# Optimization experiments

Hardware: AMD Instinct MI355X
Metric: run time of the kernel (lower is better)

The kernel has to match this reference:

```python
import jax, jax.numpy as jnp
import numpy as np

NUM_HEADS = 12
TOPK = 4


def setup_inputs() -> dict:
    key = jax.random.key(0)
    ks = jax.random.split(key, 5)
    B, N, C = 32, 577, 768
    s = 0.02
    return {
        "x": jax.random.normal(ks[0], (B, N, C), jnp.float32),
        "qkv_w": jax.random.normal(ks[1], (3 * C, C), jnp.float32) * s,
        "qkv_b": jax.random.normal(ks[2], (3 * C,), jnp.float32) * s,
        "proj_w": jax.random.normal(ks[3], (C, C), jnp.float32) * s,
        "proj_b": jax.random.normal(ks[4], (C,), jnp.float32) * s,
    }


def reference(x, qkv_w, qkv_b, proj_w, proj_b):
    B, N, C = x.shape
    H = NUM_HEADS
    D = C // H
    scale = D ** -0.5  # 0.125, matches original_attention.scale

    # qkv projection: (B,N,3C) -> (3,B,H,N,D)
    qkv = (x @ qkv_w.T + qkv_b).reshape(B, N, 3, H, D).transpose(2, 0, 3, 1, 4)
    q, k, v = qkv[0], qkv[1], qkv[2]

    # heuristic head routing: mean squared query energy per head
    scores = jnp.mean(q.astype(jnp.float32) ** 2, axis=(0, 2, 3))  # (H,)
    _, idx = jax.lax.top_k(scores, TOPK)
    idx = jnp.sort(idx)  # (topk,)

    q_sel = q[:, idx]  # (B,topk,N,D)
    k_sel = k[:, idx]
    v_sel = v[:, idx]

    attn = jax.nn.softmax(jnp.einsum('bhnd,bhmd->bhnm', q_sel, k_sel) * scale, axis=-1)
    y_sel = jnp.einsum('bhnm,bhmd->bhnd', attn, v_sel)  # (B,topk,N,D)

    # scatter selected heads back into full-size tensors (as in the torch module)
    y_full = jnp.zeros((B, H, N, D), x.dtype).at[:, idx].set(y_sel)
    x_out = y_full.transpose(0, 2, 1, 3).reshape(B, N, C) @ proj_w.T + proj_b

    attn_full = jnp.zeros((B, H, N, N), x.dtype).at[:, idx].set(attn)
    return x_out, attn_full
```

## Files before the change

### kernel.cpp

```cpp
#include <hip/hip_runtime.h>
#include <hip/hip_bf16.h>
#include <stdint.h>
#include <stddef.h>

#define B_ 32
#define N_ 577
#define C_ 768
#define H_ 12
#define D_ 64
#define M_ (B_*N_)
#define K3_ (3*C_)
#define NP_ 640
#define NN_ (N_*N_)

typedef __bf16 bf16x8_t __attribute__((ext_vector_type(8)));
typedef float f32x4 __attribute__((ext_vector_type(4)));
typedef unsigned short u16x8 __attribute__((ext_vector_type(8)));
typedef unsigned short u16x4 __attribute__((ext_vector_type(4)));

static __device__ __forceinline__ f32x4 mfma16(u16x8 a, u16x8 b, f32x4 c) {
  return __builtin_amdgcn_mfma_f32_16x16x32_bf16(
      __builtin_bit_cast(bf16x8_t, a), __builtin_bit_cast(bf16x8_t, b), c, 0, 0, 0);
}

static __device__ __forceinline__ unsigned short f2bf(float x) {
  unsigned int u = __builtin_bit_cast(unsigned int, x);
  u += 0x7fffu + ((u >> 16) & 1u);
  return (unsigned short)(u >> 16);
}

static __device__ __forceinline__ void glds16(const unsigned short* g, unsigned short* l) {
  __builtin_amdgcn_global_load_lds(
      (__attribute__((address_space(1))) void*)g,
      (__attribute__((address_space(3))) void*)l,
      16, 0, 0);
}

static __device__ __forceinline__ void top4sel(const float* __restrict__ scores, int* sel) {
  float s[H_];
  #pragma unroll
  for (int i = 0; i < H_; ++i) s[i] = scores[i];
  #pragma unroll
  for (int t = 0; t < 4; ++t) {
    int best = 0; float bv = s[0];
    #pragma unroll
    for (int i = 1; i < H_; ++i)
      if (s[i] > bv) { bv = s[i]; best = i; }
    sel[t] = best;
    #pragma unroll
    for (int i = 0; i < H_; ++i)
      s[i] = (i == best) ? -3.0e38f : s[i];
  }
  #pragma unroll
  for (int a = 0; a < 4; ++a)
    #pragma unroll
    for (int b2 = a + 1; b2 < 4; ++b2)
      if (sel[b2] < sel[a]) { int t = sel[a]; sel[a] = sel[b2]; sel[b2] = t; }
}

__global__ void k_cvt2(const float* __restrict__ srcx, unsigned short* __restrict__ dstx, int n4x,
                       const float* __restrict__ srcw, unsigned short* __restrict__ dstw, int n4w,
                       float* __restrict__ zeroptr) {
  if (blockIdx.x == 0 && threadIdx.x < 16) zeroptr[threadIdx.x] = 0.f;
  const float* src; unsigned short* dst; int n4, i0, stride;
  if (blockIdx.x < 2048) {
    src = srcx; dst = dstx; n4 = n4x;
    i0 = blockIdx.x * 256 + threadIdx.x; stride = 2048 * 256;
  } else {
    src = srcw; dst = dstw; n4 = n4w;
    i0 = (blockIdx.x - 2048) * 256 + threadIdx.x; stride = 512 * 256;
  }
  for (int i = i0; i < n4; i += stride) {
    float4 v = ((const float4*)src)[i];
    u16x4 o;
    o[0] = f2bf(v.x); o[1] = f2bf(v.y); o[2] = f2bf(v.z); o[3] = f2bf(v.w);
    *(u16x4*)(dst + (size_t)i * 4) = o;
  }
}

#define ZPER_ 146948
template<int MODE>
__global__ void k_gemm(const unsigned short* __restrict__ A,
                       const unsigned short* __restrict__ Bm,
                       const float* __restrict__ bias,
                       unsigned short* __restrict__ qb,
                       unsigned short* __restrict__ kb,
                       unsigned short* __restrict__ vb,
                       float* __restrict__ scores,
                       float* __restrict__ out,
                       int Mtot, int Ktot)
{
  __shared__ unsigned short As[128 * 32];
  __shared__ unsigned short Bs[128 * 32];
  const int tid = threadIdx.x;
  int bn;

  if (MODE == 0) {
    const int y = blockIdx.y;
    if ((y & 3) == 0) {
      const int zblk = (y >> 2) * 145 + blockIdx.x;
      const size_t Z = (size_t)B_ * H_ * NN_;
      size_t s0 = (size_t)zblk * ZPER_;
      size_t len = ZPER_;
      if (s0 + len > Z) len = Z - s0;
      float* zo = out + s0;
      const float4 z4 = {0.f, 0.f, 0.f, 0.f};
      for (size_t t = tid * 4; t + 4 <= len; t += 4096)
        *(float4*)(zo + t) = z4;
      return;
    }
    bn = y - 1 - (y >> 2);
  } else {
    bn = blockIdx.y;
  }

  const int bm = blockIdx.x;
  const int w = tid >> 6, l = tid & 63;
  const int wm = w >> 1, wn = w & 1;
  const int lr = l & 15, lg = l >> 4;
  const int lk = lg * 8;
  f32x4 acc[4][4] = {};
  const int rowA0 = bm * 128, rowB0 = bn * 128;
  const int le0 = w * 1024 + l * 8;
  const int kiters = Ktot >> 5;
  for (int kt = 0; kt < kiters; ++kt) {
    __syncthreads();
    #pragma unroll
    for (int c = 0; c < 2; ++c) {
      int lea = le0 + c * 512;
      int ra = lea >> 5, ka = lea & 31;
      glds16(A  + (size_t)(rowA0 + ra) * Ktot + kt * 32 + ka, As + (w * 2 + c) * 512);
      glds16(Bm + (size_t)(rowB0 + ra) * Ktot + kt * 32 + ka, Bs + (w * 2 + c) * 512);
    }
    __syncthreads();
    u16x8 af[4], bfr[4];
    #pragma unroll
    for (int i = 0; i < 4; ++i)
      af[i] = *(const u16x8*)(As + (wm * 64 + i * 16 + lr) * 32 + lk);
    #pragma unroll
    for (int j = 0; j < 4; ++j)
      bfr[j] = *(const u16x8*)(Bs + (wn * 64 + j * 16 + lr) * 32 + lk);
    #pragma unroll
    for (int i = 0; i < 4; ++i)
      #pragma unroll
      for (int j = 0; j < 4; ++j)
        acc[i][j] = mfma16(af[i], bfr[j], acc[i][j]);
  }

  const int rbase = lg * 4;
  if (MODE == 0) {
    const int n0 = rowB0 + wn * 64;
    const int t0 = n0 / C_;
    const int h0 = (n0 % C_) >> 6;
    unsigned short* dstbuf = (t0 == 0) ? qb : ((t0 == 1) ? kb : vb);
    float bs[4];
    #pragma unroll
    for (int j = 0; j < 4; ++j) bs[j] = bias[n0 + j * 16 + lr];
    float sq = 0.f;
    #pragma unroll
    for (int i = 0; i < 4; ++i) {
      const int mbase = rowA0 + wm * 64 + i * 16 + rbase;
      const int bb0 = mbase / N_;
      const int np0 = mbase - bb0 * N_;
      #pragma unroll
      for (int r = 0; r < 4; ++r) {
        const int mm = mbase + r;
        if (mm < Mtot) {
          int np = np0 + r, bb = bb0;
          if (np >= N_) { np -= N_; bb += 1; }
          unsigned short* drow = dstbuf + (((size_t)(bb * H_ + h0)) * N_ + np) * D_;
          #pragma unroll
          for (int j = 0; j < 4; ++j) {
            const float v = acc[i][j][r] + bs[j];
            if (t0 == 0) sq += v * v;
            drow[j * 16 + lr] = f2bf(v);
          }
        }
      }
    }
    if (t0 == 0) {
      #pragma unroll
      for (int s2 = 1; s2 < 64; s2 <<= 1) sq += __shfl_xor(sq, s2);
      if (l == 0) atomicAdd(scores + h0, sq);
    }
  } else {
    #pragma unroll
    for (int j = 0; j < 4; ++j) {
      const int n = rowB0 + wn * 64 + j * 16 + lr;
      const float bsj = bias[n];
      #pragma unroll
      for (int i = 0; i < 4; ++i) {
        const int mbase = rowA0 + wm * 64 + i * 16 + rbase;
        #pragma unroll
        for (int r = 0; r < 4; ++r) {
          const int mm = mbase + r;
          if (mm < Mtot) out[(size_t)mm * C_ + n] = acc[i][j][r] + bsj;
        }
      }
    }
  }
}

__global__ void k_prep(const unsigned short* __restrict__ vb, unsigned short* __restrict__ vT,
                       const float* __restrict__ scores,
                       const float* __restrict__ pw, unsigned short* __restrict__ pwsel) {
  int sel[4];
  top4sel(scores, sel);
  const int bid = blockIdx.x;
  const int tid = threadIdx.x;

  if (bid >= 1280) {
    const int i = (bid - 1280) * 256 + tid;
    const int c = i >> 8, j = i & 255;
    const int h = sel[j >> 6], d = j & 63;
    pwsel[i] = f2bf(pw[(size_t)c * C_ + h * 64 + d]);
    return;
  }

  __shared__ unsigned short t[64][72];
  const int nt = bid % 10;
  const int p  = bid / 10;
  const int b  = p >> 2, hs = p & 3;
  const int h  = sel[hs];
  const size_t bh_src = (size_t)(b * H_ + h);
  const size_t bh_dst = (size_t)(b * 4 + hs);
  const int n0 = nt * 64;
  {
    const int r = tid >> 2, q4 = (tid & 3) * 16;
    const int n = n0 + r;
    u16x8 v0, v1;
    if (n < N_) {
      const unsigned short* src = vb + (bh_src * N_ + n) * D_ + q4;
      v0 = *(const u16x8*)(src);
      v1 = *(const u16x8*)(src + 8);
    } else {
      #pragma unroll
      for (int j = 0; j < 8; ++j) { v0[j] = 0; v1[j] = 0; }
    }
    *(u16x8*)&t[r][q4] = v0;
    *(u16x8*)&t[r][q4 + 8] = v1;
  }
  __syncthreads();
  {
    const int d = tid >> 2, nc = (tid & 3) * 16;
    u16x8 w0, w1;
    #pragma unroll
    for (int j = 0; j < 8; ++j) { w0[j] = t[nc + j][d]; w1[j] = t[nc + 8 + j][d]; }
    unsigned short* dst = vT + (bh_dst * D_ + d) * NP_ + n0 + nc;
    *(u16x8*)(dst) = w0;
    *(u16x8*)(dst + 8) = w1;
  }
}

__global__ void k_attn(const unsigned short* __restrict__ qb,
                       const unsigned short* __restrict__ kb,
                       const unsigned short* __restrict__ vT,
                       const float* __restrict__ scores,
                       float* __restrict__ attn_out,
                       unsigned short* __restrict__ ysel)
{
  __shared__ unsigned short Plds[4][16][72];
  int sel[4];
  top4sel(scores, sel);
  const int bid = blockIdx.x;

  const int qt = bid >> 7;
  const int pair = bid & 127;
  const int b  = pair >> 2;
  const int hs = pair & 3;
  const int h  = sel[hs];
  const int tid = threadIdx.x;
  const int w = tid >> 6, l = tid & 63;
  const int lr = l & 15, lg = l >> 4, lk = lg * 8;
  const float sc2 = 0.125f * 1.44269504f;

  const size_t bh = (size_t)(b * H_ + h);
  const unsigned short* qbase = qb + bh * ((size_t)N_ * D_);
  const unsigned short* kbase = kb + bh * ((size_t)N_ * D_);
  const unsigned short* vbase = vT + (size_t)(b * 4 + hs) * ((size_t)D_ * NP_);
  float* aout = attn_out + bh * (size_t)NN_;

  const int qrow = qt * 64 + w * 16 + lr;
  const int qrc = (qrow < N_) ? qrow : (N_ - 1);
  u16x8 qf0 = *(const u16x8*)(qbase + (size_t)qrc * D_ + lk);
  u16x8 qf1 = *(const u16x8*)(qbase + (size_t)qrc * D_ + 32 + lk);

  const unsigned short* kp576 = kbase + (size_t)576 * D_;
  u16x8 kt0 = *(const u16x8*)(kp576 + lk);
  u16x8 kt1 = *(const u16x8*)(kp576 + 32 + lk);

  float lsum[4] = {0.f, 0.f, 0.f, 0.f};

  for (int kt = 0; kt < 9; ++kt) {
    f32x4 s[4];
    #pragma unroll
    for (int cg = 0; cg < 4; ++cg) {
      const int kc = kt * 64 + cg * 16 + lr;
      const unsigned short* kp = kbase + (size_t)kc * D_;
      u16x8 k0 = *(const u16x8*)(kp + lk);
      u16x8 k1 = *(const u16x8*)(kp + 32 + lk);
      f32x4 a = {0.f, 0.f, 0.f, 0.f};
      __builtin_amdgcn_s_setprio(1);
      a = mfma16(qf0, k0, a);
      a = mfma16(qf1, k1, a);
      __builtin_amdgcn_s_setprio(0);
      s[cg] = a;
    }
    #pragma unroll
    for (int r = 0; r < 4; ++r) {
      #pragma unroll
      for (int cg = 0; cg < 4; ++cg)
        lsum[r] += exp2f(s[cg][r] * sc2);
    }
  }
  {
    f32x4 a = {0.f, 0.f, 0.f, 0.f};
    a = mfma16(qf0, kt0, a);
    a = mfma16(qf1, kt1, a);
    #pragma unroll
    for (int r = 0; r < 4; ++r)
      lsum[r] += (lr == 0) ? exp2f(a[r] * sc2) : 0.f;
  }
  #pragma unroll
  for (int x = 1; x < 16; x <<= 1)
    #pragma unroll
    for (int r = 0; r < 4; ++r)
      lsum[r] += __shfl_xor(lsum[r], x);
  float off2[4];
  #pragma unroll
  for (int r = 0; r < 4; ++r) off2[r] = __log2f(lsum[r]);

  f32x4 y[4] = {};
  const int orow0 = qt * 64 + w * 16 + lg * 4;

  for (int kt = 0; kt < 9; ++kt) {
    f32x4 s[4];
    #pragma unroll
    for (int cg = 0; cg < 4; ++cg) {
      const int kc = kt * 64 + cg * 16 + lr;
      const unsigned short* kp = kbase + (size_t)kc * D_;
      u16x8 k0 = *(const u16x8*)(kp + lk);
      u16x8 k1 = *(const u16x8*)(kp + 32 + lk);
      f32x4 a = {0.f, 0.f, 0.f, 0.f};
      __builtin_amdgcn_s_setprio(1);
      a = mfma16(qf0, k0, a);
      a = mfma16(qf1, k1, a);
      __builtin_amdgcn_s_setprio(0);
      s[cg] = a;
    }
    #pragma unroll
    for (int cg = 0; cg < 4; ++cg) {
      const int kc = kt * 64 + cg * 16 + lr;
      #pragma unroll
      for (int r = 0; r < 4; ++r) {
        const float p = exp2f(__builtin_fmaf(s[cg][r], sc2, -off2[r]));
        const int row = orow0 + r;
        if (row < N_)
          aout[(size_t)row * N_ + kc] = p;
        Plds[w][lg * 4 + r][cg * 16 + lr] = f2bf(p);
      }
    }
    u16x8 pa0 = *(const u16x8*)&Plds[w][lr][lk];
    u16x8 pa1 = *(const u16x8*)&Plds[w][lr][32 + lk];
    #pragma unroll
    for (int cg2 = 0; cg2 < 4; ++cg2) {
      const unsigned short* vp = vbase + (size_t)(cg2 * 16 + lr) * NP_ + kt * 64;
      u16x8 v0 = *(const u16x8*)(vp + lk);
      u16x8 v1 = *(const u16x8*)(vp + 32 + lk);
      __builtin_amdgcn_s_setprio(1);
      y[cg2] = mfma16(pa0, v0, y[cg2]);
      y[cg2] = mfma16(pa1, v1, y[cg2]);
      __builtin_amdgcn_s_setprio(0);
    }
  }
  {
    f32x4 a = {0.f, 0.f, 0.f, 0.f};
    a = mfma16(qf0, kt0, a);
    a = mfma16(qf1, kt1, a);
    #pragma unroll
    for (int cg = 0; cg < 4; ++cg) {
      #pragma unroll
      for (int r = 0; r < 4; ++r) {
        float p = 0.f;
        if (cg == 0) {
          const float pv = exp2f(__builtin_fmaf(a[r], sc2, -off2[r]));
          p = (lr == 0) ? pv : 0.f;
          const int row = orow0 + r;
          if (lr == 0 && row < N_)
            aout[(size_t)row * N_ + 576] = pv;
        }
        Plds[w][lg * 4 + r][cg * 16 + lr] = f2bf(p);
      }
    }
    u16x8 pa0 = *(const u16x8*)&Plds[w][lr][lk];
    u16x8 pa1 = *(const u16x8*)&Plds[w][lr][32 + lk];
    #pragma unroll
    for (int cg2 = 0; cg2 < 4; ++cg2) {
      const unsigned short* vp = vbase + (size_t)(cg2 * 16 + lr) * NP_ + 576;
      u16x8 v0 = *(const u16x8*)(vp + lk);
      u16x8 v1 = *(const u16x8*)(vp + 32 + lk);
      y[cg2] = mfma16(pa0, v0, y[cg2]);
      y[cg2] = mfma16(pa1, v1, y[cg2]);
    }
  }

  #pragma unroll
  for (int cg2 = 0; cg2 < 4; ++cg2)
    #pragma unroll
    for (int r = 0; r < 4; ++r) {
      const int row = orow0 + r;
      if (row < N_)
        ysel[((size_t)(b * N_ + row)) * 256 + hs * 64 + cg2 * 16 + lr] = f2bf(y[cg2][r]);
    }
}

extern "C" void kernel_launch(void* const* d_in, const int* in_sizes, int n_in,
                              void* d_out, int out_size, void* d_ws, size_t ws_size,
                              hipStream_t stream) {
  const float* x      = (const float*)d_in[0];
  const float* qkv_w  = (const float*)d_in[1];
  const float* qkv_b  = (const float*)d_in[2];
  const float* proj_w = (const float*)d_in[3];
  const float* proj_b = (const float*)d_in[4];

  float* xout = (float*)d_out;
  float* attn_out = (float*)d_out + (size_t)M_ * C_;

  char* ws = (char*)d_ws;
  size_t o = 0;
  unsigned short* xb    = (unsigned short*)(ws + o);
  unsigned short* vT    = (unsigned short*)(ws + o);
  o += 31457280;
  unsigned short* wqkvb = (unsigned short*)(ws + o); o += 3538944;
  unsigned short* qb    = (unsigned short*)(ws + o); o += 28360704;
  unsigned short* kb    = (unsigned short*)(ws + o); o += 28360704;
  unsigned short* vb    = (unsigned short*)(ws + o); o += 28360704;
  unsigned short* ysel  = (unsigned short*)(ws + o); o += 9453568;
  unsigned short* pwsel = (unsigned short*)(ws + o); o += 393216;
  float* scores         = (float*)(ws + o);

  k_cvt2<<<2560, 256, 0, stream>>>(x, xb, (M_ * C_) / 4,
                                   qkv_w, wqkvb, (K3_ * C_) / 4, scores);

  k_gemm<0><<<dim3(145, 24), 256, 0, stream>>>(xb, wqkvb, qkv_b,
                                               qb, kb, vb, scores, attn_out,
                                               M_, C_);

  k_prep<<<2048, 256, 0, stream>>>(vb, vT, scores, proj_w, pwsel);

  k_attn<<<1280, 256, 0, stream>>>(qb, kb, vT, scores, attn_out, ysel);

  k_gemm<1><<<dim3(145, 6), 256, 0, stream>>>(ysel, pwsel, proj_b,
                                              nullptr, nullptr, nullptr, nullptr, xout,
                                              M_, 256);
}
```

Before: 358.0 us.

## Split QKV GEMM to compute K/V only for selected heads and zero only unselected attn slabs

The fused QKV GEMM now runs in two passes. The first computes only Q, because Q is needed to find the head scores. The second computes K and V only for the four selected heads, gathering their weight rows and writing compact 4-head buffers. The second pass also zeroes only the attention-map slabs of the eight unselected heads, instead of the whole attention output that the selected heads later overwrite. This removes the GEMM work for eight unselected heads' K/V and redundant zero writes, at the cost of an extra launch and a serialization point on the score reduction.

```diff
diff --git a/kernel.cpp b/kernel.cpp
--- a/kernel.cpp
+++ b/kernel.cpp
@@ -56,6 +56,10 @@
     #pragma unroll
     for (int b2 = a + 1; b2 < 4; ++b2)
       if (sel[b2] < sel[a]) { int t = sel[a]; sel[a] = sel[b2]; sel[b2] = t; }
+}
+
+static __device__ __forceinline__ int sel_pick(const int* sel, int h) {
+  return h == 0 ? sel[0] : (h == 1 ? sel[1] : (h == 2 ? sel[2] : sel[3]));
 }
 
 __global__ void k_cvt2(const float* __restrict__ srcx, unsigned short* __restrict__ dstx, int n4x,
@@ -78,7 +82,6 @@
   }
 }
 
-#define ZPER_ 146948
 template<int MODE>
 __global__ void k_gemm(const unsigned short* __restrict__ A,
                        const unsigned short* __restrict__ Bm,
@@ -94,22 +97,39 @@
   __shared__ unsigned short Bs[128 * 32];
   const int tid = threadIdx.x;
   int bn;
-
-  if (MODE == 0) {
+  int sel[4] = {0, 1, 2, 3};
+
+  if (MODE == 2) {
+    top4sel(scores, sel);
     const int y = blockIdx.y;
-    if ((y & 3) == 0) {
-      const int zblk = (y >> 2) * 145 + blockIdx.x;
-      const size_t Z = (size_t)B_ * H_ * NN_;
-      size_t s0 = (size_t)zblk * ZPER_;
-      size_t len = ZPER_;
-      if (s0 + len > Z) len = Z - s0;
-      float* zo = out + s0;
+    if (y == 0 || y == 3) {
+      const int x = blockIdx.x;
+      if (x >= 128) return;
+      const int slab = (y == 3 ? 128 : 0) + x;
+      const int b2 = slab >> 3, hu = slab & 7;
+      int uh[8]; int u = 0;
+      #pragma unroll
+      for (int c = 0; c < H_; ++c) {
+        bool issel = (c == sel[0]) | (c == sel[1]) | (c == sel[2]) | (c == sel[3]);
+        if (!issel) { uh[u] = c; ++u; }
+      }
+      int zh = 0;
+      #pragma unroll
+      for (int u2 = 0; u2 < 8; ++u2) if (u2 == hu) zh = uh[u2];
+      float* zo = out + ((size_t)(b2 * H_ + zh)) * NN_;
+      size_t take = NN_;
+      const int mis = (int)(((uintptr_t)zo >> 2) & 3);
+      size_t head = mis ? (size_t)(4 - mis) : 0;
+      if (head > take) head = take;
+      for (size_t t = tid; t < head; t += 256) zo[t] = 0.f;
+      float* pv = zo + head; size_t nrem = take - head;
+      const size_t nv = nrem >> 2;
       const float4 z4 = {0.f, 0.f, 0.f, 0.f};
-      for (size_t t = tid * 4; t + 4 <= len; t += 4096)
-        *(float4*)(zo + t) = z4;
+      for (size_t t = tid; t < nv; t += 256) ((float4*)pv)[t] = z4;
+      for (size_t t = (nv << 2) + tid; t < nrem; t += 256) pv[t] = 0.f;
       return;
     }
-    bn = y - 1 - (y >> 2);
+    bn = y - 1 - (y > 3 ? 1 : 0);
   } else {
     bn = blockIdx.y;
   }
@@ -123,6 +143,19 @@
   const int rowA0 = bm * 128, rowB0 = bn * 128;
   const int le0 = w * 1024 + l * 8;
   const int kiters = Ktot >> 5;
+
+  int brow_c[2];
+  #pragma unroll
+  for (int c = 0; c < 2; ++c) {
+    const int ra = (le0 + c * 512) >> 5;
+    int r = rowB0 + ra;
+    if (MODE == 2) {
+      const int part = r >> 8, hsr = (r >> 6) & 3, dd = r & 63;
+      r = 768 + part * 768 + sel_pick(sel, hsr) * 64 + dd;
+    }
+    brow_c[c] = r;
+  }
+
   for (int kt = 0; kt < kiters; ++kt) {
     __syncthreads();
     #pragma unroll
@@ -130,7 +163,7 @@
       int lea = le0 + c * 512;
       int ra = lea >> 5, ka = lea & 31;
       glds16(A  + (size_t)(rowA0 + ra) * Ktot + kt * 32 + ka, As + (w * 2 + c) * 512);
-      glds16(Bm + (size_t)(rowB0 + ra) * Ktot + kt * 32 + ka, Bs + (w * 2 + c) * 512);
+      glds16(Bm + (size_t)brow_c[c] * Ktot + kt * 32 + ka, Bs + (w * 2 + c) * 512);
     }
     __syncthreads();
     u16x8 af[4], bfr[4];
@@ -148,14 +181,22 @@
   }
 
   const int rbase = lg * 4;
-  if (MODE == 0) {
+  if (MODE == 0 || MODE == 2) {
     const int n0 = rowB0 + wn * 64;
-    const int t0 = n0 / C_;
-    const int h0 = (n0 % C_) >> 6;
-    unsigned short* dstbuf = (t0 == 0) ? qb : ((t0 == 1) ? kb : vb);
+    const int blk64 = n0 >> 6;
+    unsigned short* dstbuf;
+    int hcomp;
+    int bias0;
+    if (MODE == 0) {
+      dstbuf = qb; hcomp = blk64; bias0 = n0;
+    } else {
+      const int part = blk64 >> 2, hs2 = blk64 & 3;
+      dstbuf = part ? vb : kb; hcomp = hs2;
+      bias0 = 768 + part * 768 + sel_pick(sel, hs2) * 64;
+    }
     float bs[4];
     #pragma unroll
-    for (int j = 0; j < 4; ++j) bs[j] = bias[n0 + j * 16 + lr];
+    for (int j = 0; j < 4; ++j) bs[j] = bias[bias0 + j * 16 + lr];
     float sq = 0.f;
     #pragma unroll
     for (int i = 0; i < 4; ++i) {
@@ -168,20 +209,22 @@
         if (mm < Mtot) {
           int np = np0 + r, bb = bb0;
           if (np >= N_) { np -= N_; bb += 1; }
-          unsigned short* drow = dstbuf + (((size_t)(bb * H_ + h0)) * N_ + np) * D_;
+          unsigned short* drow = (MODE == 0)
+            ? dstbuf + (((size_t)(bb * H_ + hcomp)) * N_ + np) * D_
+            : dstbuf + (((size_t)(bb * 4  + hcomp)) * N_ + np) * D_;
           #pragma unroll
           for (int j = 0; j < 4; ++j) {
             const float v = acc[i][j][r] + bs[j];
-            if (t0 == 0) sq += v * v;
+            if (MODE == 0) sq += v * v;
             drow[j * 16 + lr] = f2bf(v);
           }
         }
       }
     }
-    if (t0 == 0) {
+    if (MODE == 0) {
       #pragma unroll
       for (int s2 = 1; s2 < 64; s2 <<= 1) sq += __shfl_xor(sq, s2);
-      if (l == 0) atomicAdd(scores + h0, sq);
+      if (l == 0) atomicAdd(scores + blk64, sq);
     }
   } else {
     #pragma unroll
@@ -204,15 +247,15 @@
 __global__ void k_prep(const unsigned short* __restrict__ vb, unsigned short* __restrict__ vT,
                        const float* __restrict__ scores,
                        const float* __restrict__ pw, unsigned short* __restrict__ pwsel) {
-  int sel[4];
-  top4sel(scores, sel);
   const int bid = blockIdx.x;
   const int tid = threadIdx.x;
 
   if (bid >= 1280) {
+    int sel[4];
+    top4sel(scores, sel);
     const int i = (bid - 1280) * 256 + tid;
     const int c = i >> 8, j = i & 255;
-    const int h = sel[j >> 6], d = j & 63;
+    const int h = sel_pick(sel, j >> 6), d = j & 63;
     pwsel[i] = f2bf(pw[(size_t)c * C_ + h * 64 + d]);
     return;
   }
@@ -221,16 +264,14 @@
   const int nt = bid % 10;
   const int p  = bid / 10;
   const int b  = p >> 2, hs = p & 3;
-  const int h  = sel[hs];
-  const size_t bh_src = (size_t)(b * H_ + h);
-  const size_t bh_dst = (size_t)(b * 4 + hs);
+  const size_t bh = (size_t)(b * 4 + hs);
   const int n0 = nt * 64;
   {
     const int r = tid >> 2, q4 = (tid & 3) * 16;
     const int n = n0 + r;
     u16x8 v0, v1;
     if (n < N_) {
-      const unsigned short* src = vb + (bh_src * N_ + n) * D_ + q4;
+      const unsigned short* src = vb + (bh * N_ + n) * D_ + q4;
       v0 = *(const u16x8*)(src);
       v1 = *(const u16x8*)(src + 8);
     } else {
@@ -246,7 +287,7 @@
     u16x8 w0, w1;
     #pragma unroll
     for (int j = 0; j < 8; ++j) { w0[j] = t[nc + j][d]; w1[j] = t[nc + 8 + j][d]; }
-    unsigned short* dst = vT + (bh_dst * D_ + d) * NP_ + n0 + nc;
+    unsigned short* dst = vT + (bh * D_ + d) * NP_ + n0 + nc;
     *(u16x8*)(dst) = w0;
     *(u16x8*)(dst + 8) = w1;
   }
@@ -268,17 +309,16 @@
   const int pair = bid & 127;
   const int b  = pair >> 2;
   const int hs = pair & 3;
-  const int h  = sel[hs];
+  const int h  = sel_pick(sel, hs);
   const int tid = threadIdx.x;
   const int w = tid >> 6, l = tid & 63;
   const int lr = l & 15, lg = l >> 4, lk = lg * 8;
   const float sc2 = 0.125f * 1.44269504f;
 
-  const size_t bh = (size_t)(b * H_ + h);
-  const unsigned short* qbase = qb + bh * ((size_t)N_ * D_);
-  const unsigned short* kbase = kb + bh * ((size_t)N_ * D_);
+  const unsigned short* qbase = qb + (size_t)(b * H_ + h) * ((size_t)N_ * D_);
+  const unsigned short* kbase = kb + (size_t)(b * 4 + hs) * ((size_t)N_ * D_);
   const unsigned short* vbase = vT + (size_t)(b * 4 + hs) * ((size_t)D_ * NP_);
-  float* aout = attn_out + bh * (size_t)NN_;
+  float* aout = attn_out + (size_t)(b * H_ + h) * (size_t)NN_;
 
   const int qrow = qt * 64 + w * 16 + lr;
   const int qrc = (qrow < N_) ? qrow : (N_ - 1);
@@ -442,9 +482,13 @@
   k_cvt2<<<2560, 256, 0, stream>>>(x, xb, (M_ * C_) / 4,
                                    qkv_w, wqkvb, (K3_ * C_) / 4, scores);
 
-  k_gemm<0><<<dim3(145, 24), 256, 0, stream>>>(xb, wqkvb, qkv_b,
-                                               qb, kb, vb, scores, attn_out,
-                                               M_, C_);
+  k_gemm<0><<<dim3(145, 6), 256, 0, stream>>>(xb, wqkvb, qkv_b,
+                                              qb, kb, vb, scores, nullptr,
+                                              M_, C_);
+
+  k_gemm<2><<<dim3(145, 6), 256, 0, stream>>>(xb, wqkvb, qkv_b,
+                                              qb, kb, vb, scores, attn_out,
+                                              M_, C_);
 
   k_prep<<<2048, 256, 0, stream>>>(vb, vT, scores, proj_w, pwsel);
 
```

Measured after the change: 388.7 us. +8.6%, slower.

## Zero only unselected attention heads inside attention kernel instead of during QKV GEMM

Applied to the files above, without the earlier changes.

Before, the QKV GEMM launch carried extra blocks that zeroed the whole B×H×N×N attention output, including the four selected heads that the attention kernel then overwrites. Now the attention kernel launches extra blocks that zero only the eight unselected heads per batch, which removes about a third of the redundant zero writes and takes the zeroing out of the GEMM grid. The cost is scalar, element-guarded stores instead of float4 stores in the zeroing path, and the zero traffic now competes with the attention blocks in one launch. Selected-head lookups also switch to a select chain so the sel array can stay in registers.

```diff
diff --git a/kernel.cpp b/kernel.cpp
--- a/kernel.cpp
+++ b/kernel.cpp
@@ -56,6 +56,10 @@
     #pragma unroll
     for (int b2 = a + 1; b2 < 4; ++b2)
       if (sel[b2] < sel[a]) { int t = sel[a]; sel[a] = sel[b2]; sel[b2] = t; }
+}
+
+static __device__ __forceinline__ int sel_pick(const int* sel, int h) {
+  return h == 0 ? sel[0] : (h == 1 ? sel[1] : (h == 2 ? sel[2] : sel[3]));
 }
 
 __global__ void k_cvt2(const float* __restrict__ srcx, unsigned short* __restrict__ dstx, int n4x,
@@ -78,7 +82,6 @@
   }
 }
 
-#define ZPER_ 146948
 template<int MODE>
 __global__ void k_gemm(const unsigned short* __restrict__ A,
                        const unsigned short* __restrict__ Bm,
@@ -93,27 +96,7 @@
   __shared__ unsigned short As[128 * 32];
   __shared__ unsigned short Bs[128 * 32];
   const int tid = threadIdx.x;
-  int bn;
-
-  if (MODE == 0) {
-    const int y = blockIdx.y;
-    if ((y & 3) == 0) {
-      const int zblk = (y >> 2) * 145 + blockIdx.x;
-      const size_t Z = (size_t)B_ * H_ * NN_;
-      size_t s0 = (size_t)zblk * ZPER_;
-      size_t len = ZPER_;
-      if (s0 + len > Z) len = Z - s0;
-      float* zo = out + s0;
-      const float4 z4 = {0.f, 0.f, 0.f, 0.f};
-      for (size_t t = tid * 4; t + 4 <= len; t += 4096)
-        *(float4*)(zo + t) = z4;
-      return;
-    }
-    bn = y - 1 - (y >> 2);
-  } else {
-    bn = blockIdx.y;
-  }
-
+  const int bn = blockIdx.y;
   const int bm = blockIdx.x;
   const int w = tid >> 6, l = tid & 63;
   const int wm = w >> 1, wn = w & 1;
@@ -212,7 +195,7 @@
   if (bid >= 1280) {
     const int i = (bid - 1280) * 256 + tid;
     const int c = i >> 8, j = i & 255;
-    const int h = sel[j >> 6], d = j & 63;
+    const int h = sel_pick(sel, j >> 6), d = j & 63;
     pwsel[i] = f2bf(pw[(size_t)c * C_ + h * 64 + d]);
     return;
   }
@@ -221,7 +204,7 @@
   const int nt = bid % 10;
   const int p  = bid / 10;
   const int b  = p >> 2, hs = p & 3;
-  const int h  = sel[hs];
+  const int h  = sel_pick(sel, hs);
   const size_t bh_src = (size_t)(b * H_ + h);
   const size_t bh_dst = (size_t)(b * 4 + hs);
   const int n0 = nt * 64;
@@ -252,6 +235,7 @@
   }
 }
 
+#define ZSEG_ 41617
 __global__ void k_attn(const unsigned short* __restrict__ qb,
                        const unsigned short* __restrict__ kb,
                        const unsigned short* __restrict__ vT,
@@ -263,22 +247,44 @@
   int sel[4];
   top4sel(scores, sel);
   const int bid = blockIdx.x;
+  const int tid = threadIdx.x;
+
+  if (bid >= 1280) {
+    const int zbid = bid - 1280;
+    const int seg = zbid & 7, zp = zbid >> 3;
+    const int zb = zp >> 3, hu = zp & 7;
+    int uh[8]; int u = 0;
+    #pragma unroll
+    for (int c = 0; c < H_; ++c) {
+      bool issel = (c == sel[0]) | (c == sel[1]) | (c == sel[2]) | (c == sel[3]);
+      if (!issel) { uh[u] = c; ++u; }
+    }
+    int zh = 0;
+    #pragma unroll
+    for (int u2 = 0; u2 < 8; ++u2) if (u2 == hu) zh = uh[u2];
+    float* slab = attn_out + ((size_t)(zb * H_ + zh)) * NN_ + seg * ZSEG_;
+    const int len = (seg == 7) ? (NN_ - 7 * ZSEG_) : ZSEG_;
+    for (int t = tid * 4; t < len; t += 4096) {
+      #pragma unroll
+      for (int j = 0; j < 4; ++j)
+        if (t + j < len) slab[t + j] = 0.f;
+    }
+    return;
+  }
 
   const int qt = bid >> 7;
   const int pair = bid & 127;
   const int b  = pair >> 2;
   const int hs = pair & 3;
-  const int h  = sel[hs];
-  const int tid = threadIdx.x;
+  const int h  = sel_pick(sel, hs);
   const int w = tid >> 6, l = tid & 63;
   const int lr = l & 15, lg = l >> 4, lk = lg * 8;
   const float sc2 = 0.125f * 1.44269504f;
 
-  const size_t bh = (size_t)(b * H_ + h);
-  const unsigned short* qbase = qb + bh * ((size_t)N_ * D_);
-  const unsigned short* kbase = kb + bh * ((size_t)N_ * D_);
+  const unsigned short* qbase = qb + (size_t)(b * H_ + h) * ((size_t)N_ * D_);
+  const unsigned short* kbase = kb + (size_t)(b * H_ + h) * ((size_t)N_ * D_);
   const unsigned short* vbase = vT + (size_t)(b * 4 + hs) * ((size_t)D_ * NP_);
-  float* aout = attn_out + bh * (size_t)NN_;
+  float* aout = attn_out + (size_t)(b * H_ + h) * (size_t)NN_;
 
   const int qrow = qt * 64 + w * 16 + lr;
   const int qrc = (qrow < N_) ? qrow : (N_ - 1);
@@ -442,13 +448,13 @@
   k_cvt2<<<2560, 256, 0, stream>>>(x, xb, (M_ * C_) / 4,
                                    qkv_w, wqkvb, (K3_ * C_) / 4, scores);
 
-  k_gemm<0><<<dim3(145, 24), 256, 0, stream>>>(xb, wqkvb, qkv_b,
-                                               qb, kb, vb, scores, attn_out,
+  k_gemm<0><<<dim3(145, 18), 256, 0, stream>>>(xb, wqkvb, qkv_b,
+                                               qb, kb, vb, scores, nullptr,
                                                M_, C_);
 
   k_prep<<<2048, 256, 0, stream>>>(vb, vT, scores, proj_w, pwsel);
 
-  k_attn<<<1280, 256, 0, stream>>>(qb, kb, vT, scores, attn_out, ysel);
+  k_attn<<<3328, 256, 0, stream>>>(qb, kb, vT, scores, attn_out, ysel);
 
   k_gemm<1><<<dim3(145, 6), 256, 0, stream>>>(ysel, pwsel, proj_b,
                                               nullptr, nullptr, nullptr, nullptr, xout,
```

Measured after the change: 377.4 us. +5.4%, slower.
